# Kernel optimization log

Measured on AMD Instinct MI355X. Metric: run time of the kernel, lower is better.

Reference implementation:

```python
import jax, jax.numpy as jnp
import numpy as np

HEADS, DIM_HEAD, LANDMARKS, PINV_ITERS = 8, 64, 256, 6
DIM = 512
KERNEL = 33  # residual depthwise conv kernel size (lucidrains NystromAttention default)
EPS = 1e-5   # torch LayerNorm eps


def setup_inputs() -> dict:
    key = jax.random.key(0)
    ks = jax.random.split(key, 4)
    b, n = 4, 8192  # n divisible by LANDMARKS -> no padding branch
    w = lambda k, shape: jax.random.normal(k, shape, dtype=jnp.float32) * 0.02
    return {
        "x": jax.random.normal(ks[0], (b, n, DIM), dtype=jnp.float32),
        "ln_gamma": jnp.ones((DIM,), jnp.float32),
        "ln_beta": jnp.zeros((DIM,), jnp.float32),
        "w_qkv": w(ks[1], (DIM, 3 * HEADS * DIM_HEAD)),   # to_qkv, no bias
        "w_out": w(ks[2], (HEADS * DIM_HEAD, DIM)),
        "b_out": jnp.zeros((DIM,), jnp.float32),
        "res_kernel": w(ks[3], (HEADS, 1, KERNEL, 1)),    # Conv2d(heads, heads, (33,1), groups=heads)
    }


def _moore_penrose_pinv(a, iters):
    # iterative Moore-Penrose pseudoinverse (lucidrains)
    abs_a = jnp.abs(a)
    col = abs_a.sum(-1).max()  # global max, matching torch.max(col)
    row = abs_a.sum(-2).max()
    z = jnp.swapaxes(a, -1, -2) / (col * row)
    I = jnp.eye(a.shape[-1], dtype=a.dtype)
    for _ in range(iters):
        az = a @ z
        z = 0.25 * z @ (13.0 * I - az @ (15.0 * I - az @ (7.0 * I - az)))
    return z


def reference(x, ln_gamma, ln_beta, w_qkv, w_out, b_out, res_kernel):
    b, n, d = x.shape
    h, dh, m = HEADS, DIM_HEAD, LANDMARKS
    # --- LayerNorm ---
    mu = x.mean(-1, keepdims=True)
    var = ((x - mu) ** 2).mean(-1, keepdims=True)
    xn = (x - mu) * jax.lax.rsqrt(var + EPS) * ln_gamma + ln_beta
    # --- qkv projection ---
    qkv = xn @ w_qkv                                   # (b, n, 3*h*dh)
    q, k, v = jnp.split(qkv, 3, axis=-1)
    to_heads = lambda t: t.reshape(b, n, h, dh).transpose(0, 2, 1, 3)  # (b, h, n, dh)
    q, k, v = to_heads(q), to_heads(k), to_heads(v)
    q = q * (dh ** -0.5)
    # --- landmark pooling (mean over groups of l tokens) ---
    l = n // m
    q_l = q.reshape(b, h, m, l, dh).mean(3)            # (b, h, m, dh)
    k_l = k.reshape(b, h, m, l, dh).mean(3)
    # --- three similarity matrices + softmaxes ---
    attn1 = jax.nn.softmax(jnp.einsum('bhnd,bhmd->bhnm', q, k_l), axis=-1)    # (b,h,n,m)
    attn2 = jax.nn.softmax(jnp.einsum('bhid,bhjd->bhij', q_l, k_l), axis=-1)  # (b,h,m,m)
    attn3 = jax.nn.softmax(jnp.einsum('bhmd,bhnd->bhmn', q_l, k), axis=-1)    # (b,h,m,n)
    out = (attn1 @ _moore_penrose_pinv(attn2, PINV_ITERS)) @ (attn3 @ v)      # (b,h,n,dh)
    # --- depthwise residual conv over sequence dim (groups = heads) ---
    res = jax.lax.conv_general_dilated(
        v, res_kernel, window_strides=(1, 1),
        padding=((KERNEL // 2, KERNEL // 2), (0, 0)),
        dimension_numbers=('NCHW', 'OIHW', 'NCHW'),
        feature_group_count=h)
    out = out + res
    # --- merge heads, output projection, outer residual ---
    out = out.transpose(0, 2, 1, 3).reshape(b, n, h * dh)
    att = out @ w_out + b_out
    return x + att
```

## Files before the change

kernel.cpp:

```cpp
#include <hip/hip_runtime.h>
#include <math.h>

#define NB 4
#define NSEQ 8192
#define DMODEL 512
#define NHEADS 8
#define DHEAD 64
#define NLM 256
#define LTOK 32
#define NBH 32
#define KCONV 33
#define CH3 8

typedef unsigned short bf16_t;
typedef __attribute__((ext_vector_type(8))) short bf16x8;
typedef __attribute__((ext_vector_type(4))) float f32x4;

__device__ __forceinline__ float bf2f(bf16_t u) {
  return __uint_as_float(((unsigned)u) << 16);
}
__device__ __forceinline__ bf16_t f2bf(float f) {
  unsigned u = __float_as_uint(f);
  return (bf16_t)((u + 0x7fffu + ((u >> 16) & 1u)) >> 16);
}
__device__ __forceinline__ void bfpair(unsigned u, float& lo, float& hi) {
  lo = __uint_as_float(u << 16);
  hi = __uint_as_float(u & 0xffff0000u);
}
__device__ __forceinline__ void gload16(const bf16_t* g, bf16_t* l) {
  __builtin_amdgcn_global_load_lds(
      (const __attribute__((address_space(1))) unsigned int*)g,
      (__attribute__((address_space(3))) unsigned int*)l, 16, 0, 0);
}

__global__ __launch_bounds__(256) void ln_kernel(const float* __restrict__ x,
    const float* __restrict__ gamma, const float* __restrict__ beta,
    bf16_t* __restrict__ xn) {
  int row = blockIdx.x * 4 + (threadIdx.x >> 6);
  int lane = threadIdx.x & 63;
  const float4* xr = reinterpret_cast<const float4*>(x + (size_t)row * DMODEL);
  float4 a0 = xr[lane];
  float4 a1 = xr[lane + 64];
  float s  = a0.x + a0.y + a0.z + a0.w + a1.x + a1.y + a1.z + a1.w;
  float s2 = a0.x*a0.x + a0.y*a0.y + a0.z*a0.z + a0.w*a0.w
           + a1.x*a1.x + a1.y*a1.y + a1.z*a1.z + a1.w*a1.w;
  #pragma unroll
  for (int off = 32; off; off >>= 1) {
    s  += __shfl_down(s, off);
    s2 += __shfl_down(s2, off);
  }
  s = __shfl(s, 0); s2 = __shfl(s2, 0);
  float mu = s * (1.0f / DMODEL);
  float var = s2 * (1.0f / DMODEL) - mu * mu;
  float rs = rsqrtf(var + 1e-5f);
  const float4* g4 = reinterpret_cast<const float4*>(gamma);
  const float4* b4 = reinterpret_cast<const float4*>(beta);
  float4 g0 = g4[lane], g1 = g4[lane + 64];
  float4 bb0 = b4[lane], bb1 = b4[lane + 64];
  ushort4 o0, o1;
  o0.x = f2bf((a0.x - mu) * rs * g0.x + bb0.x);
  o0.y = f2bf((a0.y - mu) * rs * g0.y + bb0.y);
  o0.z = f2bf((a0.z - mu) * rs * g0.z + bb0.z);
  o0.w = f2bf((a0.w - mu) * rs * g0.w + bb0.w);
  o1.x = f2bf((a1.x - mu) * rs * g1.x + bb1.x);
  o1.y = f2bf((a1.y - mu) * rs * g1.y + bb1.y);
  o1.z = f2bf((a1.z - mu) * rs * g1.z + bb1.z);
  o1.w = f2bf((a1.w - mu) * rs * g1.w + bb1.w);
  ushort4* o = reinterpret_cast<ushort4*>(xn + (size_t)row * DMODEL);
  o[lane] = o0; o[lane + 64] = o1;
}

__global__ void castT2_kernel(const float* __restrict__ wqkv, const float* __restrict__ wout,
                              bf16_t* __restrict__ wqkvT, bf16_t* __restrict__ woutT,
                              unsigned int* __restrict__ scal) {
  int idx = blockIdx.x * 256 + threadIdx.x;
  if (idx == 0) scal[0] = 0x3f800000u;
  if (idx == 1) scal[1] = 0u;
  if (idx < 786432) {
    int k = idx & 511, c = idx >> 9;
    float v = wqkv[(size_t)k * 1536 + c];
    if (c < 512) v *= 0.125f;
    wqkvT[idx] = f2bf(v);
  } else {
    int i = idx - 786432;
    int k = i & 511, c = i >> 9;
    woutT[i] = f2bf(wout[(size_t)k * 512 + c]);
  }
}

__global__ __launch_bounds__(256) void gemm_qkv_mfma(const bf16_t* __restrict__ A,
    const bf16_t* __restrict__ Bt, bf16_t* __restrict__ q, bf16_t* __restrict__ k,
    bf16_t* __restrict__ v) {
  __shared__ __align__(16) bf16_t As0[128 * 32];
  __shared__ __align__(16) bf16_t As1[128 * 32];
  __shared__ __align__(16) bf16_t Bs0[128 * 32];
  __shared__ __align__(16) bf16_t Bs1[128 * 32];
  int bid = blockIdx.x;
  int xcd = bid & 7;
  int idx = bid >> 3;
  int rowT = xcd * 32 + idx / 12;
  int colT = idx % 12;
  int rowB = rowT * 128, colB = colT * 128;
  int tid = threadIdx.x;
  int wave = tid >> 6, lane = tid & 63;
  int wr = (wave >> 1) * 64, wc = (wave & 1) * 64;
  int lrow = lane & 15, g = lane >> 4;
  f32x4 acc[4][4] = {};
  for (int k0 = 0; k0 < DMODEL; k0 += 64) {
    #pragma unroll
    for (int c = 0; c < 2; ++c) {
      int eb = wave * 1024 + c * 512;
      int e = eb + lane * 8;
      int r = e >> 5, cc = e & 31;
      gload16(A + (size_t)(rowB + r) * DMODEL + k0 + cc, &As0[eb]);
      gload16(A + (size_t)(rowB + r) * DMODEL + k0 + 32 + cc, &As1[eb]);
      gload16(Bt + (size_t)(colB + r) * DMODEL + k0 + cc, &Bs0[eb]);
      gload16(Bt + (size_t)(colB + r) * DMODEL + k0 + 32 + cc, &Bs1[eb]);
    }
    __syncthreads();
    #pragma unroll
    for (int ks = 0; ks < 2; ++ks) {
      const bf16_t* Ab2 = ks ? As1 : As0;
      const bf16_t* Bb2 = ks ? Bs1 : Bs0;
      bf16x8 af[4], bf[4];
      #pragma unroll
      for (int m = 0; m < 4; ++m)
        af[m] = *reinterpret_cast<const bf16x8*>(&Ab2[(wr + m * 16 + lrow) * 32 + g * 8]);
      #pragma unroll
      for (int n = 0; n < 4; ++n)
        bf[n] = *reinterpret_cast<const bf16x8*>(&Bb2[(wc + n * 16 + lrow) * 32 + g * 8]);
      #pragma unroll
      for (int m = 0; m < 4; ++m)
        #pragma unroll
        for (int n = 0; n < 4; ++n)
          acc[m][n] = __builtin_amdgcn_mfma_f32_16x16x32_bf16(af[m], bf[n], acc[m][n], 0, 0, 0);
    }
    __syncthreads();
  }
  #pragma unroll
  for (int m = 0; m < 4; ++m) {
    #pragma unroll
    for (int n = 0; n < 4; ++n) {
      int col = colB + wc + n * 16 + lrow;
      int which = col >> 9, hc = col & 511, h = hc >> 6, d = hc & 63;
      bf16_t* dst = (which == 0) ? q : (which == 1 ? k : v);
      #pragma unroll
      for (int r = 0; r < 4; ++r) {
        int row = rowB + wr + m * 16 + g * 4 + r;
        int b = row >> 13, nn = row & 8191;
        dst[((size_t)(b * NHEADS + h) * NSEQ + nn) * DHEAD + d] = f2bf(acc[m][n][r]);
      }
    }
  }
}

__global__ __launch_bounds__(256) void gemm_out_mfma(const bf16_t* __restrict__ A,
    const bf16_t* __restrict__ Bt, const float* __restrict__ bo,
    const float* __restrict__ x, float* __restrict__ y) {
  __shared__ __align__(16) bf16_t As[128 * 32];
  __shared__ __align__(16) bf16_t Bs[128 * 32];
  int rowB = blockIdx.x * 128, colB = blockIdx.y * 128;
  int tid = threadIdx.x;
  int wave = tid >> 6, lane = tid & 63;
  int wr = (wave >> 1) * 64, wc = (wave & 1) * 64;
  int lrow = lane & 15, g = lane >> 4;
  f32x4 acc[4][4] = {};
  for (int k0 = 0; k0 < DMODEL; k0 += 32) {
    #pragma unroll
    for (int c = 0; c < 2; ++c) {
      int eb = wave * 1024 + c * 512;
      int e = eb + lane * 8;
      int r = e >> 5, cc = e & 31;
      gload16(A + (size_t)(rowB + r) * DMODEL + k0 + cc, &As[eb]);
      gload16(Bt + (size_t)(colB + r) * DMODEL + k0 + cc, &Bs[eb]);
    }
    __syncthreads();
    bf16x8 af[4], bf[4];
    #pragma unroll
    for (int m = 0; m < 4; ++m)
      af[m] = *reinterpret_cast<const bf16x8*>(&As[(wr + m * 16 + lrow) * 32 + g * 8]);
    #pragma unroll
    for (int n = 0; n < 4; ++n)
      bf[n] = *reinterpret_cast<const bf16x8*>(&Bs[(wc + n * 16 + lrow) * 32 + g * 8]);
    #pragma unroll
    for (int n = 0; n < 4; ++n)
      #pragma unroll
      for (int m = 0; m < 4; ++m)
        acc[n][m] = __builtin_amdgcn_mfma_f32_16x16x32_bf16(bf[n], af[m], acc[n][m], 0, 0, 0);
    __syncthreads();
  }
  #pragma unroll
  for (int n = 0; n < 4; ++n) {
    int c0 = colB + wc + n * 16 + g * 4;
    float4 b4 = *reinterpret_cast<const float4*>(&bo[c0]);
    #pragma unroll
    for (int m = 0; m < 4; ++m) {
      int row = rowB + wr + m * 16 + lrow;
      size_t off = (size_t)row * DMODEL + c0;
      float4 xv = *reinterpret_cast<const float4*>(&x[off]);
      float4 o;
      o.x = xv.x + b4.x + acc[n][m][0];
      o.y = xv.y + b4.y + acc[n][m][1];
      o.z = xv.z + b4.z + acc[n][m][2];
      o.w = xv.w + b4.w + acc[n][m][3];
      *reinterpret_cast<float4*>(&y[off]) = o;
    }
  }
}

__global__ __launch_bounds__(256) void transpose64_kernel(const bf16_t* __restrict__ src,
    bf16_t* __restrict__ dst, int R) {
  __shared__ __align__(16) bf16_t T[64 * 64];
  int r0 = blockIdx.x * 64, bh = blockIdx.y;
  int tid = threadIdx.x;
  int jj = tid >> 2, part = tid & 3;
  const uint4* sr = reinterpret_cast<const uint4*>(
      src + ((size_t)bh * R + r0 + jj) * 64 + part * 16);
  uint4 a0 = sr[0], a1 = sr[1];
  int xr = (jj >> 3) & 7;
  int pg0 = (part * 2) ^ xr, pg1 = (part * 2 + 1) ^ xr;
  *reinterpret_cast<uint4*>(&T[jj * 64 + pg0 * 8]) = a0;
  *reinterpret_cast<uint4*>(&T[jj * 64 + pg1 * 8]) = a1;
  __syncthreads();
  int d = tid >> 2;
  unsigned ow[8];
  #pragma unroll
  for (int ee = 0; ee < 8; ++ee) {
    int n1 = part * 16 + ee * 2, n2 = n1 + 1;
    unsigned lo = T[n1 * 64 + (((d >> 3) ^ ((n1 >> 3) & 7)) * 8) + (d & 7)];
    unsigned hi = T[n2 * 64 + (((d >> 3) ^ ((n2 >> 3) & 7)) * 8) + (d & 7)];
    ow[ee] = lo | (hi << 16);
  }
  uint4* ot = reinterpret_cast<uint4*>(dst + ((size_t)bh * 64 + d) * R + r0 + part * 16);
  ot[0] = make_uint4(ow[0], ow[1], ow[2], ow[3]);
  ot[1] = make_uint4(ow[4], ow[5], ow[6], ow[7]);
}

__global__ void pool_kernel(const bf16_t* __restrict__ q, const bf16_t* __restrict__ k,
                            float* __restrict__ ql, float* __restrict__ kl,
                            bf16_t* __restrict__ qlb, bf16_t* __restrict__ klb) {
  int idx = blockIdx.x * 256 + threadIdx.x;
  const int half = NBH * NLM * DHEAD;
  const bf16_t* src = (idx < half) ? q : k;
  float* dst = (idx < half) ? ql : kl;
  bf16_t* dstb = (idx < half) ? qlb : klb;
  int i = (idx < half) ? idx : idx - half;
  int d = i & 63, m = (i >> 6) & 255, bh = i >> 14;
  const bf16_t* p = src + ((size_t)bh * NSEQ + m * LTOK) * DHEAD + d;
  float sum = 0.f;
  #pragma unroll
  for (int t = 0; t < LTOK; ++t) sum += bf2f(p[(size_t)t * DHEAD]);
  float r = sum * (1.0f / LTOK);
  dst[i] = r;
  dstb[i] = f2bf(r);
}

__global__ __launch_bounds__(256) void attn2_kernel(const float* __restrict__ ql,
    const float* __restrict__ kl, float* __restrict__ a2) {
  __shared__ float qs[64];
  __shared__ float red[256];
  int bh = blockIdx.y, i = blockIdx.x, t = threadIdx.x;
  if (t < 64) qs[t] = ql[((size_t)bh * NLM + i) * DHEAD + t];
  __syncthreads();
  const float* kr = kl + ((size_t)bh * NLM + t) * DHEAD;
  float s = 0.f;
  #pragma unroll
  for (int d = 0; d < 64; ++d) s += qs[d] * kr[d];
  red[t] = s; __syncthreads();
  for (int off = 128; off; off >>= 1) { if (t < off) red[t] = fmaxf(red[t], red[t + off]); __syncthreads(); }
  float mx = red[0]; __syncthreads();
  float p = expf(s - mx);
  red[t] = p; __syncthreads();
  for (int off = 128; off; off >>= 1) { if (t < off) red[t] += red[t + off]; __syncthreads(); }
  a2[((size_t)bh * NLM + i) * NLM + t] = p / red[0];
}

__global__ void colrow_kernel(const float* __restrict__ a2, unsigned int* __restrict__ scal) {
  int bh = blockIdx.x;
  int t = threadIdx.x;
  const float* Ab = a2 + (size_t)bh * NLM * NLM;
  float sum = 0.f;
  for (int i2 = 0; i2 < NLM; ++i2) sum += fabsf(Ab[(size_t)i2 * NLM + t]);
  __shared__ float red[256];
  red[t] = sum; __syncthreads();
  for (int off = 128; off; off >>= 1) { if (t < off) red[t] = fmaxf(red[t], red[t + off]); __syncthreads(); }
  if (t == 0) atomicMax(&scal[1], __float_as_uint(red[0]));
}

__global__ void zinit_kernel(const float* __restrict__ a2, const unsigned int* __restrict__ scal,
                             bf16_t* __restrict__ zb, bf16_t* __restrict__ a2b) {
  int idx = blockIdx.x * 256 + threadIdx.x;
  float inv = 1.0f / (__uint_as_float(scal[0]) * __uint_as_float(scal[1]));
  int j = idx & 255, i = (idx >> 8) & 255, bh = idx >> 16;
  zb[idx] = f2bf(a2[((size_t)bh * NLM + j) * NLM + i] * inv);
  a2b[idx] = f2bf(a2[idx]);
}

__global__ __launch_bounds__(256) void matmul256_b2b(bf16_t* __restrict__ C,
    const bf16_t* __restrict__ A, const bf16_t* __restrict__ Bm, float s, float alpha) {
  __shared__ __align__(16) bf16_t Ah[64][72];
  __shared__ __align__(16) bf16_t Bh[64][72];
  int bh = blockIdx.y;
  const bf16_t* Ab = A + (size_t)bh * NLM * NLM;
  const bf16_t* Bb = Bm + (size_t)bh * NLM * NLM;
  bf16_t* Cb = C + (size_t)bh * NLM * NLM;
  int rowB = (blockIdx.x >> 2) * 64, colB = (blockIdx.x & 3) * 64;
  int tid = threadIdx.x, w = tid >> 6, lane = tid & 63, tx = lane & 15, g = lane >> 4;
  int jj = tid >> 2, part = tid & 3;
  f32x4 acc[4] = {};
  for (int k0 = 0; k0 < NLM; k0 += 64) {
    {
      const uint4* ar = reinterpret_cast<const uint4*>(
          Ab + (size_t)(rowB + jj) * NLM + k0 + part * 16);
      *reinterpret_cast<uint4*>(&Ah[jj][part * 16]) = ar[0];
      *reinterpret_cast<uint4*>(&Ah[jj][part * 16 + 8]) = ar[1];
      const uint4* br = reinterpret_cast<const uint4*>(
          Bb + (size_t)(k0 + jj) * NLM + colB + part * 16);
      uint4 b0 = br[0], b1 = br[1];
      int d0 = part * 16;
      Bh[d0+ 0][jj] = (bf16_t)(b0.x & 0xffffu); Bh[d0+ 1][jj] = (bf16_t)(b0.x >> 16);
      Bh[d0+ 2][jj] = (bf16_t)(b0.y & 0xffffu); Bh[d0+ 3][jj] = (bf16_t)(b0.y >> 16);
      Bh[d0+ 4][jj] = (bf16_t)(b0.z & 0xffffu); Bh[d0+ 5][jj] = (bf16_t)(b0.z >> 16);
      Bh[d0+ 6][jj] = (bf16_t)(b0.w & 0xffffu); Bh[d0+ 7][jj] = (bf16_t)(b0.w >> 16);
      Bh[d0+ 8][jj] = (bf16_t)(b1.x & 0xffffu); Bh[d0+ 9][jj] = (bf16_t)(b1.x >> 16);
      Bh[d0+10][jj] = (bf16_t)(b1.y & 0xffffu); Bh[d0+11][jj] = (bf16_t)(b1.y >> 16);
      Bh[d0+12][jj] = (bf16_t)(b1.z & 0xffffu); Bh[d0+13][jj] = (bf16_t)(b1.z >> 16);
      Bh[d0+14][jj] = (bf16_t)(b1.w & 0xffffu); Bh[d0+15][jj] = (bf16_t)(b1.w >> 16);
    }
    __syncthreads();
    #pragma unroll
    for (int ks = 0; ks < 2; ++ks) {
      bf16x8 ah = *reinterpret_cast<const bf16x8*>(&Ah[w * 16 + tx][g * 8 + 32 * ks]);
      #pragma unroll
      for (int tn = 0; tn < 4; ++tn) {
        bf16x8 bhf = *reinterpret_cast<const bf16x8*>(&Bh[tn * 16 + tx][g * 8 + 32 * ks]);
        acc[tn] = __builtin_amdgcn_mfma_f32_16x16x32_bf16(bhf, ah, acc[tn], 0, 0, 0);
      }
    }
    __syncthreads();
  }
  int rr = rowB + w * 16 + tx;
  #pragma unroll
  for (int tn = 0; tn < 4; ++tn) {
    int c0 = colB + tn * 16 + g * 4;
    size_t off = (size_t)rr * NLM + c0;
    float a0 = 0.f, a1 = 0.f, a2v = 0.f, a3 = 0.f;
    if (s != 0.0f) {
      ushort4 av = *reinterpret_cast<const ushort4*>(&Ab[off]);
      a0 = bf2f(av.x); a1 = bf2f(av.y); a2v = bf2f(av.z); a3 = bf2f(av.w);
    }
    ushort4 o;
    o.x = f2bf(alpha * (s * a0 - acc[tn][0]));
    o.y = f2bf(alpha * (s * a1 - acc[tn][1]));
    o.z = f2bf(alpha * (s * a2v - acc[tn][2]));
    o.w = f2bf(alpha * (s * a3 - acc[tn][3]));
    *reinterpret_cast<ushort4*>(&Cb[off]) = o;
  }
}

__global__ __launch_bounds__(256) void matmul256_b2b2(
    bf16_t* __restrict__ C0, const bf16_t* __restrict__ A0,
    bf16_t* __restrict__ C1, const bf16_t* __restrict__ A1,
    const bf16_t* __restrict__ Bm, float s, float alpha) {
  __shared__ __align__(16) bf16_t Ah[64][72];
  __shared__ __align__(16) bf16_t Bh[64][72];
  int bh = blockIdx.y;
  const bf16_t* A = (blockIdx.z == 0) ? A0 : A1;
  bf16_t* C = (blockIdx.z == 0) ? C0 : C1;
  const bf16_t* Ab = A + (size_t)bh * NLM * NLM;
  const bf16_t* Bb = Bm + (size_t)bh * NLM * NLM;
  bf16_t* Cb = C + (size_t)bh * NLM * NLM;
  int rowB = (blockIdx.x >> 2) * 64, colB = (blockIdx.x & 3) * 64;
  int tid = threadIdx.x, w = tid >> 6, lane = tid & 63, tx = lane & 15, g = lane >> 4;
  int jj = tid >> 2, part = tid & 3;
  f32x4 acc[4] = {};
  for (int k0 = 0; k0 < NLM; k0 += 64) {
    {
      const uint4* ar = reinterpret_cast<const uint4*>(
          Ab + (size_t)(rowB + jj) * NLM + k0 + part * 16);
      *reinterpret_cast<uint4*>(&Ah[jj][part * 16]) = ar[0];
      *reinterpret_cast<uint4*>(&Ah[jj][part * 16 + 8]) = ar[1];
      const uint4* br = reinterpret_cast<const uint4*>(
          Bb + (size_t)(k0 + jj) * NLM + colB + part * 16);
      uint4 b0 = br[0], b1 = br[1];
      int d0 = part * 16;
      Bh[d0+ 0][jj] = (bf16_t)(b0.x & 0xffffu); Bh[d0+ 1][jj] = (bf16_t)(b0.x >> 16);
      Bh[d0+ 2][jj] = (bf16_t)(b0.y & 0xffffu); Bh[d0+ 3][jj] = (bf16_t)(b0.y >> 16);
      Bh[d0+ 4][jj] = (bf16_t)(b0.z & 0xffffu); Bh[d0+ 5][jj] = (bf16_t)(b0.z >> 16);
      Bh[d0+ 6][jj] = (bf16_t)(b0.w & 0xffffu); Bh[d0+ 7][jj] = (bf16_t)(b0.w >> 16);
      Bh[d0+ 8][jj] = (bf16_t)(b1.x & 0xffffu); Bh[d0+ 9][jj] = (bf16_t)(b1.x >> 16);
      Bh[d0+10][jj] = (bf16_t)(b1.y & 0xffffu); Bh[d0+11][jj] = (bf16_t)(b1.y >> 16);
      Bh[d0+12][jj] = (bf16_t)(b1.z & 0xffffu); Bh[d0+13][jj] = (bf16_t)(b1.z >> 16);
      Bh[d0+14][jj] = (bf16_t)(b1.w & 0xffffu); Bh[d0+15][jj] = (bf16_t)(b1.w >> 16);
    }
    __syncthreads();
    #pragma unroll
    for (int ks = 0; ks < 2; ++ks) {
      bf16x8 ah = *reinterpret_cast<const bf16x8*>(&Ah[w * 16 + tx][g * 8 + 32 * ks]);
      #pragma unroll
      for (int tn = 0; tn < 4; ++tn) {
        bf16x8 bhf = *reinterpret_cast<const bf16x8*>(&Bh[tn * 16 + tx][g * 8 + 32 * ks]);
        acc[tn] = __builtin_amdgcn_mfma_f32_16x16x32_bf16(bhf, ah, acc[tn], 0, 0, 0);
      }
    }
    __syncthreads();
  }
  int rr = rowB + w * 16 + tx;
  #pragma unroll
  for (int tn = 0; tn < 4; ++tn) {
    int c0 = colB + tn * 16 + g * 4;
    size_t off = (size_t)rr * NLM + c0;
    ushort4 av = *reinterpret_cast<const ushort4*>(&Ab[off]);
    float a0 = bf2f(av.x), a1 = bf2f(av.y), a2v = bf2f(av.z), a3 = bf2f(av.w);
    ushort4 o;
    o.x = f2bf(alpha * (s * a0 - acc[tn][0]));
    o.y = f2bf(alpha * (s * a1 - acc[tn][1]));
    o.z = f2bf(alpha * (s * a2v - acc[tn][2]));
    o.w = f2bf(alpha * (s * a3 - acc[tn][3]));
    *reinterpret_cast<ushort4*>(&Cb[off]) = o;
  }
}

__global__ __launch_bounds__(256) void matmul256_b2f(float* __restrict__ C,
    const bf16_t* __restrict__ A, const bf16_t* __restrict__ Bm, float s, float alpha) {
  __shared__ __align__(16) bf16_t Ah[64][72];
  __shared__ __align__(16) bf16_t Bh[64][72];
  int bh = blockIdx.y;
  const bf16_t* Ab = A + (size_t)bh * NLM * NLM;
  const bf16_t* Bb = Bm + (size_t)bh * NLM * NLM;
  float* Cb = C + (size_t)bh * NLM * NLM;
  int rowB = (blockIdx.x >> 2) * 64, colB = (blockIdx.x & 3) * 64;
  int tid = threadIdx.x, w = tid >> 6, lane = tid & 63, tx = lane & 15, g = lane >> 4;
  int jj = tid >> 2, part = tid & 3;
  f32x4 acc[4] = {};
  for (int k0 = 0; k0 < NLM; k0 += 64) {
    {
      const uint4* ar = reinterpret_cast<const uint4*>(
          Ab + (size_t)(rowB + jj) * NLM + k0 + part * 16);
      *reinterpret_cast<uint4*>(&Ah[jj][part * 16]) = ar[0];
      *reinterpret_cast<uint4*>(&Ah[jj][part * 16 + 8]) = ar[1];
      const uint4* br = reinterpret_cast<const uint4*>(
          Bb + (size_t)(k0 + jj) * NLM + colB + part * 16);
      uint4 b0 = br[0], b1 = br[1];
      int d0 = part * 16;
      Bh[d0+ 0][jj] = (bf16_t)(b0.x & 0xffffu); Bh[d0+ 1][jj] = (bf16_t)(b0.x >> 16);
      Bh[d0+ 2][jj] = (bf16_t)(b0.y & 0xffffu); Bh[d0+ 3][jj] = (bf16_t)(b0.y >> 16);
      Bh[d0+ 4][jj] = (bf16_t)(b0.z & 0xffffu); Bh[d0+ 5][jj] = (bf16_t)(b0.z >> 16);
      Bh[d0+ 6][jj] = (bf16_t)(b0.w & 0xffffu); Bh[d0+ 7][jj] = (bf16_t)(b0.w >> 16);
      Bh[d0+ 8][jj] = (bf16_t)(b1.x & 0xffffu); Bh[d0+ 9][jj] = (bf16_t)(b1.x >> 16);
      Bh[d0+10][jj] = (bf16_t)(b1.y & 0xffffu); Bh[d0+11][jj] = (bf16_t)(b1.y >> 16);
      Bh[d0+12][jj] = (bf16_t)(b1.z & 0xffffu); Bh[d0+13][jj] = (bf16_t)(b1.z >> 16);
      Bh[d0+14][jj] = (bf16_t)(b1.w & 0xffffu); Bh[d0+15][jj] = (bf16_t)(b1.w >> 16);
    }
    __syncthreads();
    #pragma unroll
    for (int ks = 0; ks < 2; ++ks) {
      bf16x8 ah = *reinterpret_cast<const bf16x8*>(&Ah[w * 16 + tx][g * 8 + 32 * ks]);
      #pragma unroll
      for (int tn = 0; tn < 4; ++tn) {
        bf16x8 bhf = *reinterpret_cast<const bf16x8*>(&Bh[tn * 16 + tx][g * 8 + 32 * ks]);
        acc[tn] = __builtin_amdgcn_mfma_f32_16x16x32_bf16(bhf, ah, acc[tn], 0, 0, 0);
      }
    }
    __syncthreads();
  }
  int rr = rowB + w * 16 + tx;
  #pragma unroll
  for (int tn = 0; tn < 4; ++tn) {
    int c0 = colB + tn * 16 + g * 4;
    size_t off = (size_t)rr * NLM + c0;
    float a0 = 0.f, a1 = 0.f, a2v = 0.f, a3 = 0.f;
    if (s != 0.0f) {
      ushort4 av = *reinterpret_cast<const ushort4*>(&Ab[off]);
      a0 = bf2f(av.x); a1 = bf2f(av.y); a2v = bf2f(av.z); a3 = bf2f(av.w);
    }
    float4 o;
    o.x = alpha * (s * a0 - acc[tn][0]);
    o.y = alpha * (s * a1 - acc[tn][1]);
    o.z = alpha * (s * a2v - acc[tn][2]);
    o.w = alpha * (s * a3 - acc[tn][3]);
    *reinterpret_cast<float4*>(&Cb[off]) = o;
  }
}

__global__ __launch_bounds__(256) void attn3v_mfma(const bf16_t* __restrict__ qlb,
    const bf16_t* __restrict__ k, const bf16_t* __restrict__ vT,
    float* __restrict__ Wpart, float* __restrict__ mlpart) {
  __shared__ __align__(16) bf16_t Qs0[2048], Qs1[2048];
  __shared__ __align__(16) bf16_t Ks0[2048], Ks1[2048];
  __shared__ __align__(16) bf16_t Vs0[2048], Vs1[2048];
  __shared__ __align__(16) bf16_t Ps[64][72];
  int chunk = blockIdx.x, lmt = blockIdx.y, bh = blockIdx.z;
  int tid = threadIdx.x;
  int wave = tid >> 6, lane = tid & 63;
  int w = wave, tx = lane & 15, g = lane >> 4;
  int lm0 = lmt * 64;
  const bf16_t* kb = k + (size_t)bh * NSEQ * DHEAD;
  const bf16_t* vtb = vT + (size_t)bh * DHEAD * NSEQ;
  int eb = wave * 512;
  int e = eb + lane * 8;
  int sr = e >> 5, sc = e & 31;
  {
    const bf16_t* qrow = qlb + ((size_t)bh * NLM + lm0 + sr) * DHEAD;
    gload16(qrow + sc, &Qs0[eb]);
    gload16(qrow + 32 + sc, &Qs1[eb]);
  }
  f32x4 oacc[4] = {};
  float lreg[4] = {0.f, 0.f, 0.f, 0.f};
  __syncthreads();
  bf16x8 aq0 = *reinterpret_cast<const bf16x8*>(&Qs0[(w * 16 + tx) * 32 + g * 8]);
  bf16x8 aq1 = *reinterpret_cast<const bf16x8*>(&Qs1[(w * 16 + tx) * 32 + g * 8]);
  for (int it = 0; it < NSEQ / (CH3 * 64); ++it) {
    int n0 = chunk * (NSEQ / CH3) + it * 64;
    {
      const bf16_t* krow = kb + (size_t)(n0 + sr) * DHEAD;
      gload16(krow + sc, &Ks0[eb]);
      gload16(krow + 32 + sc, &Ks1[eb]);
      const bf16_t* vrow = vtb + (size_t)sr * NSEQ + n0;
      gload16(vrow + sc, &Vs0[eb]);
      gload16(vrow + 32 + sc, &Vs1[eb]);
    }
    __syncthreads();
    f32x4 sacc[4] = {};
    #pragma unroll
    for (int tn = 0; tn < 4; ++tn) {
      bf16x8 bk0 = *reinterpret_cast<const bf16x8*>(&Ks0[(tn * 16 + tx) * 32 + g * 8]);
      bf16x8 bk1 = *reinterpret_cast<const bf16x8*>(&Ks1[(tn * 16 + tx) * 32 + g * 8]);
      sacc[tn] = __builtin_amdgcn_mfma_f32_16x16x32_bf16(aq0, bk0, sacc[tn], 0, 0, 0);
      sacc[tn] = __builtin_amdgcn_mfma_f32_16x16x32_bf16(aq1, bk1, sacc[tn], 0, 0, 0);
    }
    #pragma unroll
    for (int r = 0; r < 4; ++r) {
      float p0 = __expf(sacc[0][r]);
      float p1 = __expf(sacc[1][r]);
      float p2 = __expf(sacc[2][r]);
      float p3 = __expf(sacc[3][r]);
      float ts = p0 + p1 + p2 + p3;
      #pragma unroll
      for (int off = 1; off < 16; off <<= 1) ts += __shfl_xor(ts, off);
      lreg[r] += ts;
      int prow = w * 16 + g * 4 + r;
      Ps[prow][tx]      = f2bf(p0);
      Ps[prow][tx + 16] = f2bf(p1);
      Ps[prow][tx + 32] = f2bf(p2);
      Ps[prow][tx + 48] = f2bf(p3);
    }
    __syncthreads();
    bf16x8 ap0 = *reinterpret_cast<const bf16x8*>(&Ps[w * 16 + tx][g * 8]);
    bf16x8 ap1 = *reinterpret_cast<const bf16x8*>(&Ps[w * 16 + tx][g * 8 + 32]);
    #pragma unroll
    for (int td = 0; td < 4; ++td) {
      bf16x8 bv0 = *reinterpret_cast<const bf16x8*>(&Vs0[(td * 16 + tx) * 32 + g * 8]);
      bf16x8 bv1 = *reinterpret_cast<const bf16x8*>(&Vs1[(td * 16 + tx) * 32 + g * 8]);
      oacc[td] = __builtin_amdgcn_mfma_f32_16x16x32_bf16(bv0, ap0, oacc[td], 0, 0, 0);
      oacc[td] = __builtin_amdgcn_mfma_f32_16x16x32_bf16(bv1, ap1, oacc[td], 0, 0, 0);
    }
    __syncthreads();
  }
  size_t ob = ((size_t)(chunk * NBH + bh) * NLM + lm0 + w * 16 + tx);
  #pragma unroll
  for (int td = 0; td < 4; ++td) {
    float4 w4 = make_float4(oacc[td][0], oacc[td][1], oacc[td][2], oacc[td][3]);
    *reinterpret_cast<float4*>(&Wpart[ob * DHEAD + td * 16 + g * 4]) = w4;
  }
  if (tx == 0) {
    #pragma unroll
    for (int r = 0; r < 4; ++r) {
      size_t obr = ((size_t)(chunk * NBH + bh) * NLM + lm0 + w * 16 + g * 4 + r);
      mlpart[obr] = lreg[r];
    }
  }
}

__global__ void attn3v_combine(const float* __restrict__ Wpart,
    const float* __restrict__ mlpart, float* __restrict__ Wm) {
  int idx = blockIdx.x * 256 + threadIdx.x;
  int d = idx & 63;
  int s0 = idx >> 6;
  const int CHS = NBH * NLM;
  float L = 0.f, wv = 0.f;
  #pragma unroll
  for (int c = 0; c < CH3; ++c) {
    L += mlpart[(size_t)c * CHS + s0];
    wv += Wpart[((size_t)c * CHS + s0) * DHEAD + d];
  }
  Wm[idx] = wv / L;
}

__global__ void zw_kernel(const float* __restrict__ z, const float* __restrict__ W,
                          bf16_t* __restrict__ Ub) {
  int idx = blockIdx.x * 256 + threadIdx.x;
  int d = idx & 63, i = (idx >> 6) & 255, bh = idx >> 14;
  const float* zr = z + ((size_t)bh * NLM + i) * NLM;
  const float* Wb = W + (size_t)bh * NLM * DHEAD + d;
  float acc = 0.f;
  for (int j = 0; j < NLM; ++j) acc += zr[j] * Wb[(size_t)j * DHEAD];
  Ub[idx] = f2bf(acc);
}

__global__ __launch_bounds__(256) void attn1_mfma(const bf16_t* __restrict__ q,
    const bf16_t* __restrict__ klb, const bf16_t* __restrict__ Ut,
    bf16_t* __restrict__ outp) {
  __shared__ __align__(16) bf16_t Qs0[2048], Qs1[2048];
  __shared__ __align__(16) bf16_t Ks0[2048], Ks1[2048];
  __shared__ __align__(16) bf16_t Vs0[2048], Vs1[2048];
  __shared__ __align__(16) bf16_t Ps[64][72];
  int nt = blockIdx.x, bh = blockIdx.y;
  int tid = threadIdx.x;
  int wave = tid >> 6, lane = tid & 63;
  int w = wave, tx = lane & 15, g = lane >> 4;
  int n0 = nt * 64;
  int b = bh >> 3, h = bh & 7;
  const bf16_t* klbb = klb + (size_t)bh * NLM * DHEAD;
  const bf16_t* utb = Ut + (size_t)bh * DHEAD * NLM;
  int eb = wave * 512;
  int e = eb + lane * 8;
  int sr = e >> 5, sc = e & 31;
  {
    const bf16_t* qrow = q + ((size_t)bh * NSEQ + n0 + sr) * DHEAD;
    gload16(qrow + sc, &Qs0[eb]);
    gload16(qrow + 32 + sc, &Qs1[eb]);
  }
  f32x4 oacc[4] = {};
  float lreg[4] = {0.f, 0.f, 0.f, 0.f};
  __syncthreads();
  bf16x8 aq0 = *reinterpret_cast<const bf16x8*>(&Qs0[(w * 16 + tx) * 32 + g * 8]);
  bf16x8 aq1 = *reinterpret_cast<const bf16x8*>(&Qs1[(w * 16 + tx) * 32 + g * 8]);
  for (int it = 0; it < 4; ++it) {
    int lm0 = it * 64;
    {
      const bf16_t* krow = klbb + (size_t)(lm0 + sr) * DHEAD;
      gload16(krow + sc, &Ks0[eb]);
      gload16(krow + 32 + sc, &Ks1[eb]);
      const bf16_t* urow = utb + (size_t)sr * NLM + lm0;
      gload16(urow + sc, &Vs0[eb]);
      gload16(urow + 32 + sc, &Vs1[eb]);
    }
    __syncthreads();
    f32x4 sacc[4] = {};
    #pragma unroll
    for (int tn = 0; tn < 4; ++tn) {
      bf16x8 bk0 = *reinterpret_cast<const bf16x8*>(&Ks0[(tn * 16 + tx) * 32 + g * 8]);
      bf16x8 bk1 = *reinterpret_cast<const bf16x8*>(&Ks1[(tn * 16 + tx) * 32 + g * 8]);
      sacc[tn] = __builtin_amdgcn_mfma_f32_16x16x32_bf16(aq0, bk0, sacc[tn], 0, 0, 0);
      sacc[tn] = __builtin_amdgcn_mfma_f32_16x16x32_bf16(aq1, bk1, sacc[tn], 0, 0, 0);
    }
    #pragma unroll
    for (int r = 0; r < 4; ++r) {
      float p0 = __expf(sacc[0][r]);
      float p1 = __expf(sacc[1][r]);
      float p2 = __expf(sacc[2][r]);
      float p3 = __expf(sacc[3][r]);
      float ts = p0 + p1 + p2 + p3;
      #pragma unroll
      for (int off = 1; off < 16; off <<= 1) ts += __shfl_xor(ts, off);
      lreg[r] += ts;
      int prow = w * 16 + g * 4 + r;
      Ps[prow][tx]      = f2bf(p0);
      Ps[prow][tx + 16] = f2bf(p1);
      Ps[prow][tx + 32] = f2bf(p2);
      Ps[prow][tx + 48] = f2bf(p3);
    }
    __syncthreads();
    bf16x8 ap0 = *reinterpret_cast<const bf16x8*>(&Ps[w * 16 + tx][g * 8]);
    bf16x8 ap1 = *reinterpret_cast<const bf16x8*>(&Ps[w * 16 + tx][g * 8 + 32]);
    #pragma unroll
    for (int td = 0; td < 4; ++td) {
      bf16x8 bv0 = *reinterpret_cast<const bf16x8*>(&Vs0[(td * 16 + tx) * 32 + g * 8]);
      bf16x8 bv1 = *reinterpret_cast<const bf16x8*>(&Vs1[(td * 16 + tx) * 32 + g * 8]);
      oacc[td] = __builtin_amdgcn_mfma_f32_16x16x32_bf16(bv0, ap0, oacc[td], 0, 0, 0);
      oacc[td] = __builtin_amdgcn_mfma_f32_16x16x32_bf16(bv1, ap1, oacc[td], 0, 0, 0);
    }
    __syncthreads();
  }
  float sel = lreg[0];
  sel = ((tx & 3) == 1) ? lreg[1] : sel;
  sel = ((tx & 3) == 2) ? lreg[2] : sel;
  sel = ((tx & 3) == 3) ? lreg[3] : sel;
  float inv = 1.0f / __shfl(sel, ((tx >> 2) << 4) | (tx & 3));
  int n = n0 + w * 16 + tx;
  #pragma unroll
  for (int td = 0; td < 4; ++td) {
    ushort4 o;
    o.x = f2bf(oacc[td][0] * inv);
    o.y = f2bf(oacc[td][1] * inv);
    o.z = f2bf(oacc[td][2] * inv);
    o.w = f2bf(oacc[td][3] * inv);
    *reinterpret_cast<ushort4*>(
        &outp[((size_t)(b * NSEQ + n)) * DMODEL + h * DHEAD + td * 16 + g * 4]) = o;
  }
}

__global__ void conv_kernel(const bf16_t* __restrict__ v, const float* __restrict__ rk,
                            bf16_t* __restrict__ outp) {
  int t = blockIdx.x * 256 + threadIdx.x;
  int d8 = t & 7, h = (t >> 3) & 7, n = (t >> 6) & 8191, b = t >> 19;
  const bf16_t* vb = v + ((size_t)(b * NHEADS + h) * NSEQ) * DHEAD + d8 * 8;
  const float* wk = rk + h * KCONV;
  float a0 = 0.f, a1 = 0.f, a2 = 0.f, a3 = 0.f, a4 = 0.f, a5 = 0.f, a6 = 0.f, a7 = 0.f;
  #pragma unroll
  for (int tp = 0; tp < KCONV; ++tp) {
    int nn = n + tp - 16;
    if (nn < 0 || nn >= NSEQ) continue;
    uint4 vv = *reinterpret_cast<const uint4*>(vb + (size_t)nn * DHEAD);
    float wgt = wk[tp];
    float lo, hi;
    bfpair(vv.x, lo, hi); a0 += lo * wgt; a1 += hi * wgt;
    bfpair(vv.y, lo, hi); a2 += lo * wgt; a3 += hi * wgt;
    bfpair(vv.z, lo, hi); a4 += lo * wgt; a5 += hi * wgt;
    bfpair(vv.w, lo, hi); a6 += lo * wgt; a7 += hi * wgt;
  }
  size_t ob = ((size_t)(b * NSEQ + n)) * DMODEL + h * DHEAD + d8 * 8;
  uint4 ov = *reinterpret_cast<uint4*>(outp + ob);
  float lo, hi;
  uint4 nv;
  bfpair(ov.x, lo, hi); nv.x = ((unsigned)f2bf(lo + a0)) | (((unsigned)f2bf(hi + a1)) << 16);
  bfpair(ov.y, lo, hi); nv.y = ((unsigned)f2bf(lo + a2)) | (((unsigned)f2bf(hi + a3)) << 16);
  bfpair(ov.z, lo, hi); nv.z = ((unsigned)f2bf(lo + a4)) | (((unsigned)f2bf(hi + a5)) << 16);
  bfpair(ov.w, lo, hi); nv.w = ((unsigned)f2bf(lo + a6)) | (((unsigned)f2bf(hi + a7)) << 16);
  *reinterpret_cast<uint4*>(outp + ob) = nv;
}

extern "C" void kernel_launch(void* const* d_in, const int* in_sizes, int n_in,
                              void* d_out, int out_size, void* d_ws, size_t ws_size,
                              hipStream_t stream) {
  const float* x     = (const float*)d_in[0];
  const float* gamma = (const float*)d_in[1];
  const float* beta  = (const float*)d_in[2];
  const float* wqkv  = (const float*)d_in[3];
  const float* wout  = (const float*)d_in[4];
  const float* bout  = (const float*)d_in[5];
  const float* rk    = (const float*)d_in[6];
  float* y = (float*)d_out;

  char* wsb = (char*)d_ws;
  bf16_t* xn = (bf16_t*)(wsb);
  bf16_t* q  = (bf16_t*)(wsb + 33554432ull);
  bf16_t* k  = (bf16_t*)(wsb + 67108864ull);
  bf16_t* v  = (bf16_t*)(wsb + 100663296ull);
  float* a2f = (float*)(wsb + 134217728ull);
  bf16_t* M2b = (bf16_t*)(wsb + 134217728ull);
  bf16_t* M3b = (bf16_t*)(wsb + 138412032ull);
  bf16_t* a2b = (bf16_t*)(wsb + 150994944ull);
  bf16_t* zA  = (bf16_t*)(wsb + 155189248ull);
  bf16_t* zB  = (bf16_t*)(wsb + 159383552ull);
  bf16_t* YA  = (bf16_t*)(wsb + 163577856ull);
  bf16_t* YB  = (bf16_t*)(wsb + 167772160ull);
  float* zf  = (float*)(wsb + 150994944ull);
  float* ql  = (float*)(wsb + 176160768ull);
  float* kl  = (float*)(wsb + 178257920ull);
  float* Wm  = (float*)(wsb + 180355072ull);
  bf16_t* Ub = (bf16_t*)(wsb + 182452224ull);
  unsigned int* scal = (unsigned int*)(wsb + 184549376ull);
  bf16_t* wqkvT = (bf16_t*)(wsb + 182452224ull);
  bf16_t* woutT = (bf16_t*)(wsb + 184549440ull);
  bf16_t* qlb = (bf16_t*)(wsb + 185073728ull);
  bf16_t* klb = (bf16_t*)(wsb + 186122304ull);
  bf16_t* Ut  = (bf16_t*)(wsb + 187170880ull);

  bf16_t* vT = xn;
  float* Wpart  = (float*)(wsb + 134217728ull);
  float* mlpart = (float*)(wsb + 167772160ull);
  bf16_t* out_pre = (bf16_t*)(wsb + 134217728ull);

  castT2_kernel<<<4096, 256, 0, stream>>>(wqkv, wout, wqkvT, woutT, scal);
  ln_kernel<<<8192, 256, 0, stream>>>(x, gamma, beta, xn);
  gemm_qkv_mfma<<<3072, 256, 0, stream>>>(xn, wqkvT, q, k, v);
  transpose64_kernel<<<dim3(128, 32), 256, 0, stream>>>(v, vT, NSEQ);
  pool_kernel<<<4096, 256, 0, stream>>>(q, k, ql, kl, qlb, klb);
  attn2_kernel<<<dim3(256, 32), 256, 0, stream>>>(ql, kl, a2f);
  colrow_kernel<<<32, 256, 0, stream>>>(a2f, scal);
  zinit_kernel<<<8192, 256, 0, stream>>>(a2f, scal, zA, a2b);

  matmul256_b2b<<<dim3(16, 32), 256, 0, stream>>>(YA, a2b, zA, 0.f, -1.f);
  bf16_t *zc = zA, *zn = zB, *Yc = YA, *Yn = YB;
  for (int it = 0; it < 5; ++it) {
    matmul256_b2b<<<dim3(16, 32), 256, 0, stream>>>(M2b, Yc, Yc, 7.f, 1.f);
    matmul256_b2b<<<dim3(16, 32), 256, 0, stream>>>(M3b, Yc, M2b, 15.f, 1.f);
    matmul256_b2b2<<<dim3(16, 32, 2), 256, 0, stream>>>(zn, zc, Yn, Yc, M3b, 13.f, 0.25f);
    bf16_t* t;
    t = zc; zc = zn; zn = t;
    t = Yc; Yc = Yn; Yn = t;
  }
  matmul256_b2b<<<dim3(16, 32), 256, 0, stream>>>(M2b, Yc, Yc, 7.f, 1.f);
  matmul256_b2b<<<dim3(16, 32), 256, 0, stream>>>(M3b, Yc, M2b, 15.f, 1.f);
  matmul256_b2f<<<dim3(16, 32), 256, 0, stream>>>(zf, zc, M3b, 13.f, 0.25f);

  attn3v_mfma<<<dim3(CH3, 4, 32), 256, 0, stream>>>(qlb, k, vT, Wpart, mlpart);
  attn3v_combine<<<2048, 256, 0, stream>>>(Wpart, mlpart, Wm);
  zw_kernel<<<2048, 256, 0, stream>>>(zf, Wm, Ub);
  transpose64_kernel<<<dim3(4, 32), 256, 0, stream>>>(Ub, Ut, NLM);
  attn1_mfma<<<dim3(128, 32), 256, 0, stream>>>(q, klb, Ut, out_pre);
  conv_kernel<<<8192, 256, 0, stream>>>(v, rk, out_pre);
  gemm_out_mfma<<<dim3(256, 4), 256, 0, stream>>>(out_pre, woutT, bout, x, y);
}
```

Baseline: 621.9 us.

## Write V transposed from QKV GEMM epilogue and run conv on transposed V

The QKV GEMM epilogue now writes the V third directly in transposed (b,h,d,n) layout with 4-element vector stores, which removes the separate transpose kernel and the row-major V buffer. The residual depthwise conv is rewritten to read this transposed V. Each thread loads a contiguous window of a d-row into registers and computes 8 outputs from it, reusing the loaded values across taps. The trade-off is that the conv now does scalar 2-byte read-modify-writes to out_pre, strided across the sequence, which may coalesce poorly.

After: 601.4 us. 1.03x faster.

```diff
diff --git a/kernel.cpp b/kernel.cpp
--- a/kernel.cpp
+++ b/kernel.cpp
@@ -90,7 +90,7 @@
 
 __global__ __launch_bounds__(256) void gemm_qkv_mfma(const bf16_t* __restrict__ A,
     const bf16_t* __restrict__ Bt, bf16_t* __restrict__ q, bf16_t* __restrict__ k,
-    bf16_t* __restrict__ v) {
+    bf16_t* __restrict__ vT) {
   __shared__ __align__(16) bf16_t As0[128 * 32];
   __shared__ __align__(16) bf16_t As1[128 * 32];
   __shared__ __align__(16) bf16_t Bs0[128 * 32];
@@ -138,17 +138,32 @@
     __syncthreads();
   }
   #pragma unroll
-  for (int m = 0; m < 4; ++m) {
-    #pragma unroll
-    for (int n = 0; n < 4; ++n) {
-      int col = colB + wc + n * 16 + lrow;
-      int which = col >> 9, hc = col & 511, h = hc >> 6, d = hc & 63;
-      bf16_t* dst = (which == 0) ? q : (which == 1 ? k : v);
-      #pragma unroll
-      for (int r = 0; r < 4; ++r) {
-        int row = rowB + wr + m * 16 + g * 4 + r;
+  for (int n = 0; n < 4; ++n) {
+    int col = colB + wc + n * 16 + lrow;
+    int which = col >> 9, hc = col & 511, h = hc >> 6, d = hc & 63;
+    if (which == 2) {
+      #pragma unroll
+      for (int m = 0; m < 4; ++m) {
+        int row = rowB + wr + m * 16 + g * 4;
         int b = row >> 13, nn = row & 8191;
-        dst[((size_t)(b * NHEADS + h) * NSEQ + nn) * DHEAD + d] = f2bf(acc[m][n][r]);
+        ushort4 o;
+        o.x = f2bf(acc[m][n][0]);
+        o.y = f2bf(acc[m][n][1]);
+        o.z = f2bf(acc[m][n][2]);
+        o.w = f2bf(acc[m][n][3]);
+        *reinterpret_cast<ushort4*>(
+            &vT[((size_t)(b * NHEADS + h) * DHEAD + d) * NSEQ + nn]) = o;
+      }
+    } else {
+      bf16_t* dst = (which == 0) ? q : k;
+      #pragma unroll
+      for (int m = 0; m < 4; ++m) {
+        #pragma unroll
+        for (int r = 0; r < 4; ++r) {
+          int row = rowB + wr + m * 16 + g * 4 + r;
+          int b = row >> 13, nn = row & 8191;
+          dst[((size_t)(b * NHEADS + h) * NSEQ + nn) * DHEAD + d] = f2bf(acc[m][n][r]);
+        }
       }
     }
   }
@@ -691,34 +706,48 @@
   }
 }
 
-__global__ void conv_kernel(const bf16_t* __restrict__ v, const float* __restrict__ rk,
-                            bf16_t* __restrict__ outp) {
-  int t = blockIdx.x * 256 + threadIdx.x;
-  int d8 = t & 7, h = (t >> 3) & 7, n = (t >> 6) & 8191, b = t >> 19;
-  const bf16_t* vb = v + ((size_t)(b * NHEADS + h) * NSEQ) * DHEAD + d8 * 8;
+__global__ __launch_bounds__(256) void conv_kernel(const bf16_t* __restrict__ vT,
+    const float* __restrict__ rk, bf16_t* __restrict__ outp) {
+  int tile = blockIdx.x, bh = blockIdx.y;
+  int b = bh >> 3, h = bh & 7;
+  int tid = threadIdx.x;
+  int w = tid >> 6, d = tid & 63;
+  const bf16_t* vrow = vT + ((size_t)bh * DHEAD + d) * NSEQ;
   const float* wk = rk + h * KCONV;
-  float a0 = 0.f, a1 = 0.f, a2 = 0.f, a3 = 0.f, a4 = 0.f, a5 = 0.f, a6 = 0.f, a7 = 0.f;
-  #pragma unroll
-  for (int tp = 0; tp < KCONV; ++tp) {
-    int nn = n + tp - 16;
-    if (nn < 0 || nn >= NSEQ) continue;
-    uint4 vv = *reinterpret_cast<const uint4*>(vb + (size_t)nn * DHEAD);
-    float wgt = wk[tp];
-    float lo, hi;
-    bfpair(vv.x, lo, hi); a0 += lo * wgt; a1 += hi * wgt;
-    bfpair(vv.y, lo, hi); a2 += lo * wgt; a3 += hi * wgt;
-    bfpair(vv.z, lo, hi); a4 += lo * wgt; a5 += hi * wgt;
-    bfpair(vv.w, lo, hi); a6 += lo * wgt; a7 += hi * wgt;
-  }
-  size_t ob = ((size_t)(b * NSEQ + n)) * DMODEL + h * DHEAD + d8 * 8;
-  uint4 ov = *reinterpret_cast<uint4*>(outp + ob);
-  float lo, hi;
-  uint4 nv;
-  bfpair(ov.x, lo, hi); nv.x = ((unsigned)f2bf(lo + a0)) | (((unsigned)f2bf(hi + a1)) << 16);
-  bfpair(ov.y, lo, hi); nv.y = ((unsigned)f2bf(lo + a2)) | (((unsigned)f2bf(hi + a3)) << 16);
-  bfpair(ov.z, lo, hi); nv.z = ((unsigned)f2bf(lo + a4)) | (((unsigned)f2bf(hi + a5)) << 16);
-  bfpair(ov.w, lo, hi); nv.w = ((unsigned)f2bf(lo + a6)) | (((unsigned)f2bf(hi + a7)) << 16);
-  *reinterpret_cast<uint4*>(outp + ob) = nv;
+  int nbase = tile * 256 + w * 64;
+  for (int i = 0; i < 8; ++i) {
+    int ns = nbase + i * 8;
+    int lo = ns - 16;
+    __attribute__((aligned(16))) unsigned wv[20];
+    if (lo >= 0 && ns + 24 <= NSEQ) {
+      #pragma unroll
+      for (int u = 0; u < 5; ++u)
+        *reinterpret_cast<uint4*>(&wv[u * 4]) =
+            *reinterpret_cast<const uint4*>(vrow + lo + u * 8);
+    } else {
+      #pragma unroll
+      for (int u = 0; u < 20; ++u) {
+        int n0e = lo + u * 2, n1e = n0e + 1;
+        unsigned l16 = (n0e >= 0 && n0e < NSEQ) ? (unsigned)vrow[n0e] : 0u;
+        unsigned h16 = (n1e >= 0 && n1e < NSEQ) ? (unsigned)vrow[n1e] : 0u;
+        wv[u] = l16 | (h16 << 16);
+      }
+    }
+    #pragma unroll
+    for (int j = 0; j < 8; ++j) {
+      float acc = 0.f;
+      #pragma unroll
+      for (int t = 0; t < KCONV; ++t) {
+        int ix = j + t;
+        unsigned word = wv[ix >> 1];
+        float xv = __uint_as_float((ix & 1) ? (word & 0xffff0000u) : (word << 16));
+        acc += wk[t] * xv;
+      }
+      int n = ns + j;
+      size_t ob = ((size_t)(b * NSEQ + n)) * DMODEL + h * DHEAD + d;
+      outp[ob] = f2bf(bf2f(outp[ob]) + acc);
+    }
+  }
 }
 
 extern "C" void kernel_launch(void* const* d_in, const int* in_sizes, int n_in,
@@ -737,7 +766,7 @@
   bf16_t* xn = (bf16_t*)(wsb);
   bf16_t* q  = (bf16_t*)(wsb + 33554432ull);
   bf16_t* k  = (bf16_t*)(wsb + 67108864ull);
-  bf16_t* v  = (bf16_t*)(wsb + 100663296ull);
+  bf16_t* vT = (bf16_t*)(wsb + 100663296ull);
   float* a2f = (float*)(wsb + 134217728ull);
   bf16_t* M2b = (bf16_t*)(wsb + 134217728ull);
   bf16_t* M3b = (bf16_t*)(wsb + 138412032ull);
@@ -758,15 +787,13 @@
   bf16_t* klb = (bf16_t*)(wsb + 186122304ull);
   bf16_t* Ut  = (bf16_t*)(wsb + 187170880ull);
 
-  bf16_t* vT = xn;
   float* Wpart  = (float*)(wsb + 134217728ull);
   float* mlpart = (float*)(wsb + 167772160ull);
   bf16_t* out_pre = (bf16_t*)(wsb + 134217728ull);
 
   castT2_kernel<<<4096, 256, 0, stream>>>(wqkv, wout, wqkvT, woutT, scal);
   ln_kernel<<<8192, 256, 0, stream>>>(x, gamma, beta, xn);
-  gemm_qkv_mfma<<<3072, 256, 0, stream>>>(xn, wqkvT, q, k, v);
-  transpose64_kernel<<<dim3(128, 32), 256, 0, stream>>>(v, vT, NSEQ);
+  gemm_qkv_mfma<<<3072, 256, 0, stream>>>(xn, wqkvT, q, k, vT);
   pool_kernel<<<4096, 256, 0, stream>>>(q, k, ql, kl, qlb, klb);
   attn2_kernel<<<dim3(256, 32), 256, 0, stream>>>(ql, kl, a2f);
   colrow_kernel<<<32, 256, 0, stream>>>(a2f, scal);
@@ -791,6 +818,6 @@
   zw_kernel<<<2048, 256, 0, stream>>>(zf, Wm, Ub);
   transpose64_kernel<<<dim3(4, 32), 256, 0, stream>>>(Ub, Ut, NLM);
   attn1_mfma<<<dim3(128, 32), 256, 0, stream>>>(q, klb, Ut, out_pre);
-  conv_kernel<<<8192, 256, 0, stream>>>(v, rk, out_pre);
+  conv_kernel<<<dim3(32, 32), 256, 0, stream>>>(vT, rk, out_pre);
   gemm_out_mfma<<<dim3(256, 4), 256, 0, stream>>>(out_pre, woutT, bout, x, y);
 }
```
